# Kernel tuning notes

Hardware: AMD Instinct MI355X
Metric: run time of the kernel (lower is better)

The kernel has to match this reference:

```python
import jax, jax.numpy as jnp
import numpy as np

QB = 127.0      # 2**(bits_act-1) - 1 for bits_act=8
EPS = 1e-5

def act_quant_ste(x):
    # per-tensor int8 absmax quantization (per_token_act=False), straight-through
    scale = QB / jnp.maximum(jnp.max(jnp.abs(x)), EPS)
    q = jnp.clip(jnp.round(x * scale), -QB, QB) / scale
    return x + jax.lax.stop_gradient(q - x)

def weight_quant_ste(w):
    # BitNet b1.58 ternary quantization: scale = mean(|W|)
    beta = jnp.maximum(jnp.mean(jnp.abs(w)), EPS)
    q = jnp.clip(jnp.round(w / beta), -1.0, 1.0) * beta
    return w + jax.lax.stop_gradient(q - w)

def layernorm(x, w, b):
    mu = jnp.mean(x, axis=-1, keepdims=True)
    var = jnp.mean(jnp.square(x - mu), axis=-1, keepdims=True)
    return (x - mu) * jax.lax.rsqrt(var + EPS) * w + b

def bitlinear(x, w):
    return jnp.einsum('bsd,fd->bsf', act_quant_ste(x), weight_quant_ste(w))

def setup_inputs() -> dict:
    key = jax.random.key(0)
    k1, k2, k3 = jax.random.split(key, 3)
    d_model, d_ff = 2048, 8192
    B, S = 4, 2048
    x = jax.random.normal(k1, (B, S, d_model), dtype=jnp.float32)
    ln_w = jnp.ones((d_model,), dtype=jnp.float32)
    ln_b = jnp.zeros((d_model,), dtype=jnp.float32)
    w1 = jax.random.normal(k2, (d_ff, d_model), dtype=jnp.float32) * (1.0 / np.sqrt(d_model))
    w2 = jax.random.normal(k3, (d_model, d_ff), dtype=jnp.float32) * (1.0 / np.sqrt(d_ff))
    return {"x": x, "ln_w": ln_w, "ln_b": ln_b, "w1": w1, "w2": w2}

def reference(x, ln_w, ln_b, w1, w2):
    x_ln = layernorm(x, ln_w, ln_b)             # Sub-LN before quantized linear
    h = jax.nn.gelu(bitlinear(x_ln, w1), approximate=False)  # F.gelu default = exact
    y = bitlinear(h, w2)
    return y
```

## Files before the change

kernel.cpp:

```cpp
#include <hip/hip_runtime.h>

typedef signed char char8v __attribute__((ext_vector_type(8)));
typedef signed char char4v __attribute__((ext_vector_type(4)));
typedef short short8 __attribute__((ext_vector_type(8)));
typedef int int32x4 __attribute__((ext_vector_type(4)));

static constexpr int DM = 2048;
static constexpr int DF = 8192;
static constexpr int MT = 8192;
static constexpr int CH = 4096;
static constexpr float INVN = 1.0f / 16777216.0f;

static constexpr size_t OFF_STATS = 256;
static constexpr size_t OFF_QX   = OFF_STATS + 65536;
static constexpr size_t OFF_QW1  = OFF_QX  + (size_t)MT * DM;
static constexpr size_t OFF_QW2  = OFF_QW1 + (size_t)DF * DM;
static constexpr size_t OFF_HACC = OFF_QW2 + (size_t)DM * DF;

__device__ __forceinline__ float waveSum(float v) {
#pragma unroll
  for (int o = 32; o > 0; o >>= 1) v += __shfl_xor(v, o, 64);
  return v;
}
__device__ __forceinline__ float waveMax(float v) {
#pragma unroll
  for (int o = 32; o > 0; o >>= 1) v = fmaxf(v, __shfl_xor(v, o, 64));
  return v;
}
__device__ __forceinline__ float gelu_exact(float v) {
  return 0.5f * v * (1.0f + erff(v * 0.70710678118654752f));
}
__device__ __forceinline__ signed char q8(float v, float lo, float hi) {
  return (signed char)fminf(fmaxf(rintf(v), lo), hi);
}

__global__ __launch_bounds__(64) void zero_k(float* p) { p[threadIdx.x] = 0.f; }

__global__ __launch_bounds__(256) void abssum_k(const float4* __restrict__ w, int n4,
                                                float* __restrict__ out) {
  float s = 0.f;
  for (int i = blockIdx.x * 256 + threadIdx.x; i < n4; i += gridDim.x * 256) {
    float4 v = w[i];
    s += fabsf(v.x) + fabsf(v.y) + fabsf(v.z) + fabsf(v.w);
  }
  s = waveSum(s);
  __shared__ float sm[4];
  if ((threadIdx.x & 63) == 0) sm[threadIdx.x >> 6] = s;
  __syncthreads();
  if (threadIdx.x == 0) atomicAdd(out, sm[0] + sm[1] + sm[2] + sm[3]);
}

__global__ __launch_bounds__(256) void ln_k(const float* __restrict__ x, const float* __restrict__ w,
                                            const float* __restrict__ b, float* __restrict__ stats,
                                            unsigned* __restrict__ amax) {
  __shared__ float sm[4];
  const int row = blockIdx.x, t = threadIdx.x;
  const float4* xr = (const float4*)(x + (size_t)row * DM);
  float4 v0 = xr[t], v1 = xr[t + 256];
  float s = v0.x + v0.y + v0.z + v0.w + v1.x + v1.y + v1.z + v1.w;
  s = waveSum(s);
  if ((t & 63) == 0) sm[t >> 6] = s;
  __syncthreads();
  const float mu = (sm[0] + sm[1] + sm[2] + sm[3]) * (1.0f / DM);
  __syncthreads();
  float d[8] = {v0.x - mu, v0.y - mu, v0.z - mu, v0.w - mu,
                v1.x - mu, v1.y - mu, v1.z - mu, v1.w - mu};
  float sq = 0.f;
#pragma unroll
  for (int i = 0; i < 8; i++) sq += d[i] * d[i];
  sq = waveSum(sq);
  if ((t & 63) == 0) sm[t >> 6] = sq;
  __syncthreads();
  const float var = (sm[0] + sm[1] + sm[2] + sm[3]) * (1.0f / DM);
  const float rstd = 1.0f / sqrtf(var + 1e-5f);
  __syncthreads();
  const float4* wr = (const float4*)w;
  const float4* br = (const float4*)b;
  float4 w0 = wr[t], w1v = wr[t + 256], b0 = br[t], b1v = br[t + 256];
  float m = 0.f;
  m = fmaxf(m, fabsf(d[0] * rstd * w0.x + b0.x));
  m = fmaxf(m, fabsf(d[1] * rstd * w0.y + b0.y));
  m = fmaxf(m, fabsf(d[2] * rstd * w0.z + b0.z));
  m = fmaxf(m, fabsf(d[3] * rstd * w0.w + b0.w));
  m = fmaxf(m, fabsf(d[4] * rstd * w1v.x + b1v.x));
  m = fmaxf(m, fabsf(d[5] * rstd * w1v.y + b1v.y));
  m = fmaxf(m, fabsf(d[6] * rstd * w1v.z + b1v.z));
  m = fmaxf(m, fabsf(d[7] * rstd * w1v.w + b1v.w));
  m = waveMax(m);
  if ((t & 63) == 0) sm[t >> 6] = m;
  __syncthreads();
  if (t == 0) {
    float mm = fmaxf(fmaxf(sm[0], sm[1]), fmaxf(sm[2], sm[3]));
    stats[2 * row] = mu;
    stats[2 * row + 1] = rstd;
    atomicMax(amax, __float_as_uint(mm));
  }
}

__global__ __launch_bounds__(256) void quantx_k(const float* __restrict__ x, const float* __restrict__ w,
                                                const float* __restrict__ b, const float* __restrict__ stats,
                                                const float* __restrict__ scal, signed char* __restrict__ qx) {
  const int row = blockIdx.x, t = threadIdx.x;
  const float mu = stats[2 * row], rstd = stats[2 * row + 1];
  const float sc = 127.0f / fmaxf(scal[2], 1e-5f);
  const float4* xr = (const float4*)(x + (size_t)row * DM);
  const float4* wr = (const float4*)w;
  const float4* br = (const float4*)b;
  float4 v0 = xr[2 * t], v1 = xr[2 * t + 1];
  float4 w0 = wr[2 * t], w1v = wr[2 * t + 1];
  float4 b0 = br[2 * t], b1v = br[2 * t + 1];
  char8v o;
  o[0] = q8(((v0.x - mu) * rstd * w0.x + b0.x) * sc, -127.f, 127.f);
  o[1] = q8(((v0.y - mu) * rstd * w0.y + b0.y) * sc, -127.f, 127.f);
  o[2] = q8(((v0.z - mu) * rstd * w0.z + b0.z) * sc, -127.f, 127.f);
  o[3] = q8(((v0.w - mu) * rstd * w0.w + b0.w) * sc, -127.f, 127.f);
  o[4] = q8(((v1.x - mu) * rstd * w1v.x + b1v.x) * sc, -127.f, 127.f);
  o[5] = q8(((v1.y - mu) * rstd * w1v.y + b1v.y) * sc, -127.f, 127.f);
  o[6] = q8(((v1.z - mu) * rstd * w1v.z + b1v.z) * sc, -127.f, 127.f);
  o[7] = q8(((v1.w - mu) * rstd * w1v.w + b1v.w) * sc, -127.f, 127.f);
  *(char8v*)(qx + (size_t)row * DM + t * 8) = o;
}

__global__ __launch_bounds__(256) void quantw_k(const float4* __restrict__ w, const float* __restrict__ sumabs,
                                                signed char* __restrict__ qw, int n4) {
  const float beta = fmaxf(*sumabs * INVN, 1e-5f);
  const float rb = 1.0f / beta;
  for (int i = blockIdx.x * 256 + threadIdx.x; i < n4; i += gridDim.x * 256) {
    float4 v = w[i];
    char4v o;
    o[0] = q8(v.x * rb, -1.f, 1.f);
    o[1] = q8(v.y * rb, -1.f, 1.f);
    o[2] = q8(v.z * rb, -1.f, 1.f);
    o[3] = q8(v.w * rb, -1.f, 1.f);
    *(char4v*)(qw + (size_t)i * 4) = o;
  }
}

__global__ __launch_bounds__(256) void quanth_k(const short8* __restrict__ hacc,
                                                const float* __restrict__ scal,
                                                signed char* __restrict__ qh, int n8) {
  const float s1 = fmaxf(scal[0] * INVN, 1e-5f) * fmaxf(scal[2], 1e-5f) * (1.0f / 127.0f);
  const float sc2 = 127.0f / fmaxf(scal[3], 1e-5f);
  for (int i = blockIdx.x * 256 + threadIdx.x; i < n8; i += gridDim.x * 256) {
    short8 v = hacc[i];
    char8v o;
#pragma unroll
    for (int j = 0; j < 8; j++) {
      const float g = gelu_exact((float)v[j] * s1);
      o[j] = q8(g * sc2, -127.f, 127.f);
    }
    *(char8v*)(qh + (size_t)i * 8) = o;
  }
}

__device__ __forceinline__ void gll16(const signed char* g, signed char* l) {
  __builtin_amdgcn_global_load_lds((const __attribute__((address_space(1))) void*)g,
                                   (__attribute__((address_space(3))) void*)l, 16, 0, 0);
}

template <int EPI>
__global__ __launch_bounds__(256, 4) void gemm_i8(const signed char* __restrict__ A,
                                                  const signed char* __restrict__ B,
                                                  void* __restrict__ Cv, int M, int N, int K, int nbx,
                                                  const float* __restrict__ p_sumw,
                                                  const float* __restrict__ p_amax,
                                                  unsigned* __restrict__ amax_out) {
  __shared__ signed char As[128 * 64];
  __shared__ signed char Bs[128 * 64];
  const int tid = threadIdx.x;
  const int wid = tid >> 6, lane = tid & 63;

  const int nwg = gridDim.x;
  const int qc = nwg >> 3;
  const int swz = ((int)blockIdx.x & 7) * qc + ((int)blockIdx.x >> 3);
  const int bx = swz % nbx, by = swz / nbx;
  const int m0 = by * 128, n0 = bx * 128;
  const int wm = (wid >> 1) * 64, wn = (wid & 1) * 64;

  int32x4 acc[4][4];
#pragma unroll
  for (int i = 0; i < 4; i++)
#pragma unroll
    for (int j = 0; j < 4; j++) acc[i][j] = int32x4{0, 0, 0, 0};

  const int srow = tid >> 2;
  const int scol = (tid & 3) * 16;
  const signed char* gA = A + (size_t)(m0 + srow) * K + scol;
  const signed char* gB = B + (size_t)(n0 + srow) * K + scol;
  const size_t rowK64 = (size_t)64 * K;

  const int lrow = lane & 15;
  const int lkb = (lane >> 4) * 16;
  const int aoff = (wm + lrow) * 64 + lkb;
  const int boff = (wn + lrow) * 64 + lkb;

  for (int k0 = 0; k0 < K; k0 += 64) {
    __syncthreads();
    gll16(gA + k0,          As + wid * 1024);
    gll16(gA + k0 + rowK64, As + 4096 + wid * 1024);
    gll16(gB + k0,          Bs + wid * 1024);
    gll16(gB + k0 + rowK64, Bs + 4096 + wid * 1024);
    __syncthreads();

    int32x4 af[4], bfv[4];
#pragma unroll
    for (int m = 0; m < 4; m++) af[m] = *(const int32x4*)(As + aoff + m * 1024);
#pragma unroll
    for (int n = 0; n < 4; n++) bfv[n] = *(const int32x4*)(Bs + boff + n * 1024);
#pragma unroll
    for (int m = 0; m < 4; m++)
#pragma unroll
      for (int n = 0; n < 4; n++)
        acc[m][n] = __builtin_amdgcn_mfma_i32_16x16x64_i8(af[m], bfv[n], acc[m][n], 0, 0, 0);
  }

  const float beta = fmaxf(p_sumw[0] * INVN, 1e-5f);
  const float s = beta * fmaxf(p_amax[0], 1e-5f) * (1.0f / 127.0f);
  const int crow0 = m0 + wm + ((lane >> 4) << 2);
  const int ccol0 = n0 + wn + (lane & 15);
  float lmax = 0.f;
#pragma unroll
  for (int m = 0; m < 4; m++) {
#pragma unroll
    for (int n = 0; n < 4; n++) {
#pragma unroll
      for (int j = 0; j < 4; j++) {
        const float a = (float)acc[m][n][j];
        const size_t idx = (size_t)(crow0 + m * 16 + j) * N + (ccol0 + n * 16);
        if (EPI == 1) {
          ((short*)Cv)[idx] = (short)fminf(fmaxf(a, -32767.f), 32767.f);
          lmax = fmaxf(lmax, fabsf(gelu_exact(a * s)));
        } else {
          ((float*)Cv)[idx] = a * s;
        }
      }
    }
  }
  if (EPI == 1) {
    lmax = waveMax(lmax);
    if (lane == 0) atomicMax(amax_out, __float_as_uint(lmax));
  }
}

extern "C" void kernel_launch(void* const* d_in, const int* in_sizes, int n_in,
                              void* d_out, int out_size, void* d_ws, size_t ws_size,
                              hipStream_t stream) {
  const float* x = (const float*)d_in[0];
  const float* lnw = (const float*)d_in[1];
  const float* lnb = (const float*)d_in[2];
  const float* w1 = (const float*)d_in[3];
  const float* w2 = (const float*)d_in[4];
  float* out = (float*)d_out;

  char* ws = (char*)d_ws;
  float* scal = (float*)ws;
  float* stats = (float*)(ws + OFF_STATS);
  signed char* qx = (signed char*)(ws + OFF_QX);
  signed char* qw1 = (signed char*)(ws + OFF_QW1);
  signed char* qw2 = (signed char*)(ws + OFF_QW2);
  short* hacc = (short*)(ws + OFF_HACC);
  signed char* qh = (signed char*)(ws + OFF_QX);

  zero_k<<<1, 64, 0, stream>>>(scal);
  abssum_k<<<2048, 256, 0, stream>>>((const float4*)w1, (DF * DM) / 4, &scal[0]);
  abssum_k<<<2048, 256, 0, stream>>>((const float4*)w2, (DM * DF) / 4, &scal[1]);
  ln_k<<<MT, 256, 0, stream>>>(x, lnw, lnb, stats, (unsigned*)&scal[2]);
  quantx_k<<<MT, 256, 0, stream>>>(x, lnw, lnb, stats, scal, qx);
  quantw_k<<<2048, 256, 0, stream>>>((const float4*)w1, &scal[0], qw1, (DF * DM) / 4);
  quantw_k<<<2048, 256, 0, stream>>>((const float4*)w2, &scal[1], qw2, (DM * DF) / 4);

  gemm_i8<1><<<dim3((DF / 128) * (MT / 128)), 256, 0, stream>>>(qx, qw1, hacc, MT, DF, DM, DF / 128,
                                                                &scal[0], &scal[2], (unsigned*)&scal[3]);
  for (int c = 0; c < MT / CH; c++) {
    quanth_k<<<2048, 256, 0, stream>>>((const short8*)(hacc + (size_t)c * CH * DF), scal,
                                       qh, (CH * DF) / 8);
    gemm_i8<0><<<dim3((DM / 128) * (CH / 128)), 256, 0, stream>>>(qh, qw2, out + (size_t)c * CH * DM,
                                                                  CH, DM, DF, DM / 128,
                                                                  &scal[1], &scal[3], nullptr);
  }
}
```

Baseline: 984.7 us.

## Use double-precision weight abs-sum and band-based XCD tile mapping for GEMMs

Weight absolute sums are now accumulated in double precision with double atomics, so the ternary scale is more exact. The GEMM block-to-tile mapping also changes: each XCD gets a contiguous band of M rows and walks across N, where before the swizzle spread a linear tile order over XCDs. The new mapping is meant to improve L2 reuse of A rows within each XCD, at the cost of possibly less B reuse. The double reductions add a small amount of FP64 work to the reduction kernels.

Result: no change. 966.3 us (-1.9%).

```diff
diff --git a/kernel.cpp b/kernel.cpp
--- a/kernel.cpp
+++ b/kernel.cpp
@@ -9,7 +9,7 @@
 static constexpr int DF = 8192;
 static constexpr int MT = 8192;
 static constexpr int CH = 4096;
-static constexpr float INVN = 1.0f / 16777216.0f;
+static constexpr double INVND = 1.0 / 16777216.0;
 
 static constexpr size_t OFF_STATS = 256;
 static constexpr size_t OFF_QX   = OFF_STATS + 65536;
@@ -22,6 +22,11 @@
   for (int o = 32; o > 0; o >>= 1) v += __shfl_xor(v, o, 64);
   return v;
 }
+__device__ __forceinline__ double waveSumD(double v) {
+#pragma unroll
+  for (int o = 32; o > 0; o >>= 1) v += __shfl_xor(v, o, 64);
+  return v;
+}
 __device__ __forceinline__ float waveMax(float v) {
 #pragma unroll
   for (int o = 32; o > 0; o >>= 1) v = fmaxf(v, __shfl_xor(v, o, 64));
@@ -37,14 +42,14 @@
 __global__ __launch_bounds__(64) void zero_k(float* p) { p[threadIdx.x] = 0.f; }
 
 __global__ __launch_bounds__(256) void abssum_k(const float4* __restrict__ w, int n4,
-                                                float* __restrict__ out) {
-  float s = 0.f;
+                                                double* __restrict__ out) {
+  double s = 0.0;
   for (int i = blockIdx.x * 256 + threadIdx.x; i < n4; i += gridDim.x * 256) {
     float4 v = w[i];
-    s += fabsf(v.x) + fabsf(v.y) + fabsf(v.z) + fabsf(v.w);
-  }
-  s = waveSum(s);
-  __shared__ float sm[4];
+    s += (double)fabsf(v.x) + (double)fabsf(v.y) + (double)fabsf(v.z) + (double)fabsf(v.w);
+  }
+  s = waveSumD(s);
+  __shared__ double sm[4];
   if ((threadIdx.x & 63) == 0) sm[threadIdx.x >> 6] = s;
   __syncthreads();
   if (threadIdx.x == 0) atomicAdd(out, sm[0] + sm[1] + sm[2] + sm[3]);
@@ -99,10 +104,10 @@
 
 __global__ __launch_bounds__(256) void quantx_k(const float* __restrict__ x, const float* __restrict__ w,
                                                 const float* __restrict__ b, const float* __restrict__ stats,
-                                                const float* __restrict__ scal, signed char* __restrict__ qx) {
+                                                const float* __restrict__ fam, signed char* __restrict__ qx) {
   const int row = blockIdx.x, t = threadIdx.x;
   const float mu = stats[2 * row], rstd = stats[2 * row + 1];
-  const float sc = 127.0f / fmaxf(scal[2], 1e-5f);
+  const float sc = 127.0f / fmaxf(fam[0], 1e-5f);
   const float4* xr = (const float4*)(x + (size_t)row * DM);
   const float4* wr = (const float4*)w;
   const float4* br = (const float4*)b;
@@ -121,9 +126,10 @@
   *(char8v*)(qx + (size_t)row * DM + t * 8) = o;
 }
 
-__global__ __launch_bounds__(256) void quantw_k(const float4* __restrict__ w, const float* __restrict__ sumabs,
+__global__ __launch_bounds__(256) void quantw_k(const float4* __restrict__ w,
+                                                const double* __restrict__ sumabs,
                                                 signed char* __restrict__ qw, int n4) {
-  const float beta = fmaxf(*sumabs * INVN, 1e-5f);
+  const float beta = fmaxf((float)(sumabs[0] * INVND), 1e-5f);
   const float rb = 1.0f / beta;
   for (int i = blockIdx.x * 256 + threadIdx.x; i < n4; i += gridDim.x * 256) {
     float4 v = w[i];
@@ -137,10 +143,12 @@
 }
 
 __global__ __launch_bounds__(256) void quanth_k(const short8* __restrict__ hacc,
-                                                const float* __restrict__ scal,
+                                                const double* __restrict__ dsum,
+                                                const float* __restrict__ fam,
                                                 signed char* __restrict__ qh, int n8) {
-  const float s1 = fmaxf(scal[0] * INVN, 1e-5f) * fmaxf(scal[2], 1e-5f) * (1.0f / 127.0f);
-  const float sc2 = 127.0f / fmaxf(scal[3], 1e-5f);
+  const float beta = fmaxf((float)(dsum[0] * INVND), 1e-5f);
+  const float s1 = beta * fmaxf(fam[0], 1e-5f) * (1.0f / 127.0f);
+  const float sc2 = 127.0f / fmaxf(fam[1], 1e-5f);
   for (int i = blockIdx.x * 256 + threadIdx.x; i < n8; i += gridDim.x * 256) {
     short8 v = hacc[i];
     char8v o;
@@ -161,8 +169,9 @@
 template <int EPI>
 __global__ __launch_bounds__(256, 4) void gemm_i8(const signed char* __restrict__ A,
                                                   const signed char* __restrict__ B,
-                                                  void* __restrict__ Cv, int M, int N, int K, int nbx,
-                                                  const float* __restrict__ p_sumw,
+                                                  void* __restrict__ Cv, int M, int N, int K,
+                                                  int bandrows,
+                                                  const double* __restrict__ p_sumw,
                                                   const float* __restrict__ p_amax,
                                                   unsigned* __restrict__ amax_out) {
   __shared__ signed char As[128 * 64];
@@ -170,10 +179,10 @@
   const int tid = threadIdx.x;
   const int wid = tid >> 6, lane = tid & 63;
 
-  const int nwg = gridDim.x;
-  const int qc = nwg >> 3;
-  const int swz = ((int)blockIdx.x & 7) * qc + ((int)blockIdx.x >> 3);
-  const int bx = swz % nbx, by = swz / nbx;
+  const int xcd = (int)blockIdx.x & 7;
+  const int idx = (int)blockIdx.x >> 3;
+  const int by = xcd * bandrows + (idx % bandrows);
+  const int bx = idx / bandrows;
   const int m0 = by * 128, n0 = bx * 128;
   const int wm = (wid >> 1) * 64, wn = (wid & 1) * 64;
 
@@ -214,7 +223,7 @@
         acc[m][n] = __builtin_amdgcn_mfma_i32_16x16x64_i8(af[m], bfv[n], acc[m][n], 0, 0, 0);
   }
 
-  const float beta = fmaxf(p_sumw[0] * INVN, 1e-5f);
+  const float beta = fmaxf((float)(p_sumw[0] * INVND), 1e-5f);
   const float s = beta * fmaxf(p_amax[0], 1e-5f) * (1.0f / 127.0f);
   const int crow0 = m0 + wm + ((lane >> 4) << 2);
   const int ccol0 = n0 + wn + (lane & 15);
@@ -226,12 +235,12 @@
 #pragma unroll
       for (int j = 0; j < 4; j++) {
         const float a = (float)acc[m][n][j];
-        const size_t idx = (size_t)(crow0 + m * 16 + j) * N + (ccol0 + n * 16);
+        const size_t idx2 = (size_t)(crow0 + m * 16 + j) * N + (ccol0 + n * 16);
         if (EPI == 1) {
-          ((short*)Cv)[idx] = (short)fminf(fmaxf(a, -32767.f), 32767.f);
+          ((short*)Cv)[idx2] = (short)fminf(fmaxf(a, -32767.f), 32767.f);
           lmax = fmaxf(lmax, fabsf(gelu_exact(a * s)));
         } else {
-          ((float*)Cv)[idx] = a * s;
+          ((float*)Cv)[idx2] = a * s;
         }
       }
     }
@@ -253,7 +262,8 @@
   float* out = (float*)d_out;
 
   char* ws = (char*)d_ws;
-  float* scal = (float*)ws;
+  double* dsum = (double*)ws;
+  float* fam = (float*)(ws + 16);
   float* stats = (float*)(ws + OFF_STATS);
   signed char* qx = (signed char*)(ws + OFF_QX);
   signed char* qw1 = (signed char*)(ws + OFF_QW1);
@@ -261,21 +271,22 @@
   short* hacc = (short*)(ws + OFF_HACC);
   signed char* qh = (signed char*)(ws + OFF_QX);
 
-  zero_k<<<1, 64, 0, stream>>>(scal);
-  abssum_k<<<2048, 256, 0, stream>>>((const float4*)w1, (DF * DM) / 4, &scal[0]);
-  abssum_k<<<2048, 256, 0, stream>>>((const float4*)w2, (DM * DF) / 4, &scal[1]);
-  ln_k<<<MT, 256, 0, stream>>>(x, lnw, lnb, stats, (unsigned*)&scal[2]);
-  quantx_k<<<MT, 256, 0, stream>>>(x, lnw, lnb, stats, scal, qx);
-  quantw_k<<<2048, 256, 0, stream>>>((const float4*)w1, &scal[0], qw1, (DF * DM) / 4);
-  quantw_k<<<2048, 256, 0, stream>>>((const float4*)w2, &scal[1], qw2, (DM * DF) / 4);
-
-  gemm_i8<1><<<dim3((DF / 128) * (MT / 128)), 256, 0, stream>>>(qx, qw1, hacc, MT, DF, DM, DF / 128,
-                                                                &scal[0], &scal[2], (unsigned*)&scal[3]);
+  zero_k<<<1, 64, 0, stream>>>((float*)ws);
+  abssum_k<<<2048, 256, 0, stream>>>((const float4*)w1, (DF * DM) / 4, &dsum[0]);
+  abssum_k<<<2048, 256, 0, stream>>>((const float4*)w2, (DM * DF) / 4, &dsum[1]);
+  ln_k<<<MT, 256, 0, stream>>>(x, lnw, lnb, stats, (unsigned*)&fam[0]);
+  quantx_k<<<MT, 256, 0, stream>>>(x, lnw, lnb, stats, fam, qx);
+  quantw_k<<<2048, 256, 0, stream>>>((const float4*)w1, &dsum[0], qw1, (DF * DM) / 4);
+  quantw_k<<<2048, 256, 0, stream>>>((const float4*)w2, &dsum[1], qw2, (DM * DF) / 4);
+
+  gemm_i8<1><<<dim3((DF / 128) * (MT / 128)), 256, 0, stream>>>(qx, qw1, hacc, MT, DF, DM,
+                                                                MT / 128 / 8, &dsum[0], &fam[0],
+                                                                (unsigned*)&fam[1]);
   for (int c = 0; c < MT / CH; c++) {
-    quanth_k<<<2048, 256, 0, stream>>>((const short8*)(hacc + (size_t)c * CH * DF), scal,
+    quanth_k<<<2048, 256, 0, stream>>>((const short8*)(hacc + (size_t)c * CH * DF), &dsum[0], fam,
                                        qh, (CH * DF) / 8);
     gemm_i8<0><<<dim3((DM / 128) * (CH / 128)), 256, 0, stream>>>(qh, qw2, out + (size_t)c * CH * DM,
-                                                                  CH, DM, DF, DM / 128,
-                                                                  &scal[1], &scal[3], nullptr);
-  }
-}
+                                                                  CH, DM, DF, CH / 128 / 8,
+                                                                  &dsum[1], &fam[1], nullptr);
+  }
+}
```
